# Performance work log

Measured on AMD Instinct MI355X. Metric: run time of the kernel, lower is better.

Reference implementation:

```python
import jax, jax.numpy as jnp
import numpy as np
import math

B, S, HID = 2, 2048, 2048
H, HK, D = 16, 4, 128          # query heads, kv heads, head_dim
R = 64                         # rope_dim = head_dim * partial_rotary_factor
EPS = 1e-6
THETA = 10000.0


def _rope_tables():
    inv_freq = 1.0 / (THETA ** (np.arange(0, R, 2, dtype=np.float32) / R))
    t = np.arange(S, dtype=np.float32)
    freqs = np.outer(t, inv_freq)                      # [S, R/2]
    emb = np.concatenate([freqs, freqs], axis=-1)      # [S, R]
    cos = np.broadcast_to(np.cos(emb)[None], (B, S, R)).copy()
    sin = np.broadcast_to(np.sin(emb)[None], (B, S, R)).copy()
    return jnp.asarray(cos), jnp.asarray(sin)


def setup_inputs() -> dict:
    key = jax.random.key(0)
    ks = jax.random.split(key, 3)
    cos, sin = _rope_tables()
    return {
        "hidden_states": jax.random.normal(ks[0], (B, S, HID), dtype=jnp.float32),
        "cos": cos,
        "sin": sin,
        "w_qkv": jax.random.normal(ks[1], ((H + 2 * HK) * D, HID), dtype=jnp.float32) * (HID ** -0.5),
        "q_ln_w": jnp.ones((D,), dtype=jnp.float32),
        "k_ln_w": jnp.ones((D,), dtype=jnp.float32),
        "w_dense": jax.random.normal(ks[2], (HID, H * D), dtype=jnp.float32) * ((H * D) ** -0.5),
    }


def _rms_norm(x, w):
    xf = x.astype(jnp.float32)
    var = jnp.mean(xf * xf, axis=-1, keepdims=True)
    return w * (xf * jax.lax.rsqrt(var + EPS)).astype(x.dtype)


def _rotate_half(x):
    x1, x2 = x[..., : x.shape[-1] // 2], x[..., x.shape[-1] // 2 :]
    return jnp.concatenate([-x2, x1], axis=-1)


def _apply_rope(q, k, cos, sin):
    # cos/sin: [B, S, R] -> [B, 1, S, R]; partial rotary on first R dims
    cos = cos[:, None, :, :]
    sin = sin[:, None, :, :]
    q_rot, q_pass = q[..., :R], q[..., R:]
    k_rot, k_pass = k[..., :R], k[..., R:]
    q_emb = q_rot * cos + _rotate_half(q_rot) * sin
    k_emb = k_rot * cos + _rotate_half(k_rot) * sin
    return (jnp.concatenate([q_emb, q_pass], axis=-1),
            jnp.concatenate([k_emb, k_pass], axis=-1))


def reference(hidden_states, cos, sin, w_qkv, q_ln_w, k_ln_w, w_dense):
    bsz, q_len, _ = hidden_states.shape
    qkv = jnp.einsum('bsh,oh->bso', hidden_states, w_qkv)            # [B,S,(H+2HK)*D]
    qkv = qkv.reshape(bsz, q_len, H + 2 * HK, D)
    q, k, v = jnp.split(qkv, [H, H + HK], axis=2)
    q = jnp.transpose(q, (0, 2, 1, 3))                               # [B,H,S,D]
    k = jnp.transpose(k, (0, 2, 1, 3))                               # [B,HK,S,D]
    v = jnp.transpose(v, (0, 2, 1, 3))

    q = _rms_norm(q, q_ln_w)
    k = _rms_norm(k, k_ln_w)
    q, k = _apply_rope(q, k, cos, sin)

    n_rep = H // HK
    k = jnp.repeat(k, n_rep, axis=1)                                 # [B,H,S,D]
    v = jnp.repeat(v, n_rep, axis=1)

    scores = jnp.einsum('bhqd,bhkd->bhqk', q, k) / math.sqrt(D)
    probs = jax.nn.softmax(scores.astype(jnp.float32), axis=-1).astype(q.dtype)
    attn = jnp.einsum('bhqk,bhkd->bhqd', probs, v)                   # [B,H,S,D]
    attn = jnp.transpose(attn, (0, 2, 1, 3)).reshape(bsz, q_len, H * D)
    return jnp.einsum('bsd,od->bso', attn, w_dense)                  # [B,S,HID]
```

## Files before the change

kernel.cpp:

```cpp
#include <hip/hip_runtime.h>
#include <hip/hip_bf16.h>
#include <math.h>

#define B_   2
#define S_   2048
#define HID_ 2048
#define H_   16
#define HK_  4
#define D_   128
#define NH_  24
#define QKVN 3072
#define R_   64

typedef __attribute__((ext_vector_type(8))) _Float16 h8;
typedef __attribute__((ext_vector_type(4))) _Float16 h4;
typedef __attribute__((ext_vector_type(2))) _Float16 h2;
typedef __attribute__((ext_vector_type(4))) float f4;

#define GLOAD16(gp, lp) __builtin_amdgcn_global_load_lds(                      \
    (const __attribute__((address_space(1))) void*)(gp),                       \
    (__attribute__((address_space(3))) void*)(lp), 16, 0, 0)

__global__ __launch_bounds__(256) void cvt3(
    const float* __restrict__ s0, _Float16* __restrict__ d0, int n0,
    const float* __restrict__ s1, _Float16* __restrict__ d1, int n1,
    const float* __restrict__ s2, _Float16* __restrict__ d2, int n2)
{
    int j = blockIdx.x * 256 + threadIdx.x;
    const float* s; _Float16* d;
    if (j < n0) { s = s0; d = d0; }
    else {
        j -= n0;
        if (j < n1) { s = s1; d = d1; }
        else { j -= n1; if (j >= n2) return; s = s2; d = d2; }
    }
    float4 a = ((const float4*)s)[j * 2];
    float4 b = ((const float4*)s)[j * 2 + 1];
    h8 h;
    h[0] = (_Float16)a.x; h[1] = (_Float16)a.y;
    h[2] = (_Float16)a.z; h[3] = (_Float16)a.w;
    h[4] = (_Float16)b.x; h[5] = (_Float16)b.y;
    h[6] = (_Float16)b.z; h[7] = (_Float16)b.w;
    ((h8*)d)[j] = h;
}

__global__ __launch_bounds__(256) void gemm_qkv(
    const _Float16* __restrict__ A, const _Float16* __restrict__ Bm,
    const float* __restrict__ cosT, const float* __restrict__ sinT,
    const float* __restrict__ qw, const float* __restrict__ kw,
    _Float16* __restrict__ Qh_g, _Float16* __restrict__ Kh_g,
    _Float16* __restrict__ Vt_g)
{
    __shared__ _Float16 smem[2][128][64];
    __shared__ float exch[2][128];
    auto Ast = smem[0];
    auto Bst = smem[1];

    const int tid = threadIdx.x;
    const int wave = tid >> 6, lane = tid & 63;
    const int l15 = lane & 15, l4 = lane >> 4;
    const int h  = blockIdx.x;
    const int m0 = blockIdx.y * 128;
    const int n0 = h * 128;
    const int wm = (wave >> 1) * 64, wn = (wave & 1) * 64;
    const int K = HID_;

    f4 acc[16];
#pragma unroll
    for (int t = 0; t < 16; ++t) acc[t] = (f4){0.f, 0.f, 0.f, 0.f};

    const int srow = lane >> 3;
    const int scol = ((lane & 7) ^ srow) * 8;
    const int sw   = l15 & 7;

    for (int k0 = 0; k0 < K; k0 += 64) {
        __syncthreads();
#pragma unroll
        for (int t = 0; t < 4; ++t) {
            const int chunk = wave * 4 + t;
            const int grow  = chunk * 8 + srow;
            GLOAD16(A  + (size_t)(m0 + grow) * K + k0 + scol, &Ast[chunk * 8][0]);
            GLOAD16(Bm + (size_t)(n0 + grow) * K + k0 + scol, &Bst[chunk * 8][0]);
        }
        __syncthreads();

#pragma unroll
        for (int j = 0; j < 2; ++j) {
            h8 ahf[4], bhf[4];
#pragma unroll
            for (int i = 0; i < 4; ++i) {
                ahf[i] = *(const h8*)&Ast[wm + i * 16 + l15][((j * 4 + l4) ^ sw) * 8];
                bhf[i] = *(const h8*)&Bst[wn + i * 16 + l15][((j * 4 + l4) ^ sw) * 8];
            }
            __builtin_amdgcn_s_setprio(1);
#pragma unroll
            for (int i = 0; i < 4; ++i)
#pragma unroll
                for (int jj = 0; jj < 4; ++jj)
                    acc[i * 4 + jj] = __builtin_amdgcn_mfma_f32_16x16x32_f16(
                        ahf[i], bhf[jj], acc[i * 4 + jj], 0, 0, 0);
            __builtin_amdgcn_s_setprio(0);
        }
    }

    const int bb = m0 >> 11;
    const int s0 = m0 & 2047;

    if (h < 20) {
        float sq[4][4];
#pragma unroll
        for (int i = 0; i < 4; ++i)
#pragma unroll
            for (int r = 0; r < 4; ++r) {
                float s = 0.f;
#pragma unroll
                for (int jj = 0; jj < 4; ++jj) {
                    float v = acc[i * 4 + jj][r];
                    s += v * v;
                }
                s += __shfl_xor(s, 1);
                s += __shfl_xor(s, 2);
                s += __shfl_xor(s, 4);
                s += __shfl_xor(s, 8);
                sq[i][r] = s;
            }
        const int half = wn >> 6;
        if (l15 == 0) {
#pragma unroll
            for (int i = 0; i < 4; ++i)
#pragma unroll
                for (int r = 0; r < 4; ++r)
                    exch[half][wm + i * 16 + l4 * 4 + r] = sq[i][r];
        }
        __syncthreads();

        const float* wln = (h < 16) ? qw : kw;
        float wv[4];
#pragma unroll
        for (int jj = 0; jj < 4; ++jj) wv[jj] = wln[wn + jj * 16 + l15];

        const float QS = 0.08838834764831845f * 1.4426950408889634f;
        _Float16 (*Ld)[128] = (_Float16 (*)[128])smem;

#pragma unroll
        for (int i = 0; i < 4; ++i) {
#pragma unroll
            for (int r = 0; r < 4; ++r) {
                const int row = wm + i * 16 + l4 * 4 + r;
                const int s  = s0 + row;
                float tot = sq[i][r] + exch[half ^ 1][row];
                float scale = rsqrtf(tot * (1.f / 128.f) + 1e-6f);
                float y[4];
#pragma unroll
                for (int jj = 0; jj < 4; ++jj)
                    y[jj] = acc[i * 4 + jj][r] * scale * wv[jj];

                float yr[4];
                if (wn == 0) {
                    const float* cp = cosT + ((size_t)bb * S_ + s) * R_;
                    const float* sp = sinT + ((size_t)bb * S_ + s) * R_;
                    float cs[4], sn[4];
#pragma unroll
                    for (int jj = 0; jj < 4; ++jj) {
                        cs[jj] = cp[jj * 16 + l15];
                        sn[jj] = sp[jj * 16 + l15];
                    }
                    yr[0] = y[0] * cs[0] - y[2] * sn[0];
                    yr[1] = y[1] * cs[1] - y[3] * sn[1];
                    yr[2] = y[2] * cs[2] + y[0] * sn[2];
                    yr[3] = y[3] * cs[3] + y[1] * sn[3];
                } else {
#pragma unroll
                    for (int jj = 0; jj < 4; ++jj) yr[jj] = y[jj];
                }

                const float os = (h < 16) ? QS : 1.f;
#pragma unroll
                for (int jj = 0; jj < 4; ++jj)
                    Ld[row][wn + jj * 16 + l15] = (_Float16)(yr[jj] * os);
            }
        }
        __syncthreads();

        _Float16* outb = (h < 16)
            ? Qh_g + (((size_t)bb * H_ + h) * S_ + s0) * D_
            : Kh_g + (((size_t)bb * HK_ + (h - 16)) * S_ + s0) * D_;
        const int rr = tid >> 4;
        const int d0 = (tid & 15) * 8;
#pragma unroll
        for (int it = 0; it < 8; ++it) {
            const int row = it * 16 + rr;
            *(h8*)(outb + (size_t)row * D_ + d0) = *(const h8*)&Ld[row][d0];
        }
    } else {
        const size_t vbase = ((size_t)bb * HK_ + (h - 20)) * D_ * S_;
#pragma unroll
        for (int i = 0; i < 4; ++i)
#pragma unroll
            for (int jj = 0; jj < 4; ++jj) {
                h4 pk;
#pragma unroll
                for (int r = 0; r < 4; ++r) pk[r] = (_Float16)acc[i * 4 + jj][r];
                const int d = wn + jj * 16 + l15;
                const int s = s0 + wm + i * 16 + l4 * 4;
                *(h4*)(Vt_g + vbase + (size_t)d * S_ + s) = pk;
            }
    }
}

__global__ __launch_bounds__(256) void gemm_dense(
    const _Float16* __restrict__ A, const _Float16* __restrict__ Bm,
    float* __restrict__ Cv, int M, int N, int K)
{
    __shared__ _Float16 Ast[128][64];
    __shared__ _Float16 Bst[128][64];

    const int tid = threadIdx.x;
    const int wave = tid >> 6, lane = tid & 63;
    const int l15 = lane & 15, l4 = lane >> 4;
    const int m0 = blockIdx.y * 128, n0 = blockIdx.x * 128;
    const int wm = (wave >> 1) * 64, wn = (wave & 1) * 64;

    f4 acc[16];
#pragma unroll
    for (int t = 0; t < 16; ++t) acc[t] = (f4){0.f, 0.f, 0.f, 0.f};

    const int srow = lane >> 3;
    const int scol = ((lane & 7) ^ srow) * 8;
    const int sw   = l15 & 7;

    for (int k0 = 0; k0 < K; k0 += 64) {
        __syncthreads();
#pragma unroll
        for (int t = 0; t < 4; ++t) {
            const int chunk = wave * 4 + t;
            const int grow  = chunk * 8 + srow;
            GLOAD16(A  + (size_t)(m0 + grow) * K + k0 + scol, &Ast[chunk * 8][0]);
            GLOAD16(Bm + (size_t)(n0 + grow) * K + k0 + scol, &Bst[chunk * 8][0]);
        }
        __syncthreads();

#pragma unroll
        for (int j = 0; j < 2; ++j) {
            h8 ahf[4], bhf[4];
#pragma unroll
            for (int i = 0; i < 4; ++i) {
                ahf[i] = *(const h8*)&Ast[wm + i * 16 + l15][((j * 4 + l4) ^ sw) * 8];
                bhf[i] = *(const h8*)&Bst[wn + i * 16 + l15][((j * 4 + l4) ^ sw) * 8];
            }
            __builtin_amdgcn_s_setprio(1);
#pragma unroll
            for (int i = 0; i < 4; ++i)
#pragma unroll
                for (int jj = 0; jj < 4; ++jj)
                    acc[i * 4 + jj] = __builtin_amdgcn_mfma_f32_16x16x32_f16(
                        ahf[i], bhf[jj], acc[i * 4 + jj], 0, 0, 0);
            __builtin_amdgcn_s_setprio(0);
        }
    }

#pragma unroll
    for (int i = 0; i < 4; ++i)
#pragma unroll
        for (int jj = 0; jj < 4; ++jj)
#pragma unroll
            for (int r = 0; r < 4; ++r) {
                int row = m0 + wm + i * 16 + l4 * 4 + r;
                int col = n0 + wn + jj * 16 + l15;
                Cv[(size_t)row * N + col] = acc[i * 4 + jj][r];
            }
}

__global__ __launch_bounds__(256, 2) void flash_mfma(
    const _Float16* __restrict__ Qh_g, const _Float16* __restrict__ Kh_g,
    const _Float16* __restrict__ Vt_g, _Float16* __restrict__ Ao, int bbase)
{
    __shared__ _Float16 Ksh[2][64][128];
    __shared__ _Float16 Vsh[2][128][64];
    __shared__ _Float16 Ps [128][64];

    const int tid = threadIdx.x;
    const int wave = tid >> 6, lane = tid & 63;
    const int l15 = lane & 15, l4 = lane >> 4;
    const int qb = blockIdx.x, h = blockIdx.y, b = bbase;
    const int kh = h >> 2;
    const int key = l15 & 7;

    h8 qf[2][4];
#pragma unroll
    for (int i = 0; i < 2; ++i) {
        const _Float16* qrow = Qh_g +
            (((size_t)b * H_ + h) * S_ + qb * 128 + wave * 32 + i * 16 + l15) * D_;
#pragma unroll
        for (int j = 0; j < 4; ++j)
            qf[i][j] = *(const h8*)(qrow + j * 32 + l4 * 8);
    }

    f4 o[2][8];
#pragma unroll
    for (int i = 0; i < 2; ++i)
#pragma unroll
        for (int t = 0; t < 8; ++t) o[i][t] = (f4){0.f, 0.f, 0.f, 0.f};
    float l_part[2] = {0.f, 0.f};

    const size_t kvoff = ((size_t)b * HK_ + kh) * S_ * D_;
    const _Float16* kg = Kh_g + kvoff;
    const _Float16* vg = Vt_g + kvoff;

    int krow[4], ksrc[4], vrow[4], vsrc[4];
#pragma unroll
    for (int t = 0; t < 4; ++t) {
        krow[t] = wave * 16 + t * 4 + (lane >> 4);
        ksrc[t] = ((lane & 15) ^ (krow[t] & 7)) * 8;
        vrow[t] = wave * 32 + t * 8 + (lane >> 3);
        vsrc[t] = ((lane & 7) ^ (vrow[t] & 7)) * 8;
    }

    auto STAGE = [&](int bf, int kb) {
#pragma unroll
        for (int t = 0; t < 4; ++t)
            GLOAD16(kg + (size_t)(kb * 64 + krow[t]) * D_ + ksrc[t],
                    &Ksh[bf][wave * 16 + t * 4][0]);
#pragma unroll
        for (int t = 0; t < 4; ++t)
            GLOAD16(vg + (size_t)vrow[t] * S_ + kb * 64 + vsrc[t],
                    &Vsh[bf][wave * 32 + t * 8][0]);
    };

    STAGE(0, 0);
    int cur = 0;

    for (int kb = 0; kb < S_ / 64; ++kb) {
        __syncthreads();
        if (kb + 1 < S_ / 64) STAGE(cur ^ 1, kb + 1);

        f4 acc[4][2];
#pragma unroll
        for (int c = 0; c < 4; ++c)
#pragma unroll
            for (int i = 0; i < 2; ++i)
                acc[c][i] = (f4){-8.f, -8.f, -8.f, -8.f};
#pragma unroll
        for (int j = 0; j < 4; ++j) {
#pragma unroll
            for (int c = 0; c < 4; ++c) {
                h8 kf = *(const h8*)&Ksh[cur][c * 16 + l15][((j * 4 + l4) ^ key) * 8];
#pragma unroll
                for (int i = 0; i < 2; ++i)
                    acc[c][i] = __builtin_amdgcn_mfma_f32_16x16x32_f16(
                        kf, qf[i][j], acc[c][i], 0, 0, 0);
            }
        }

#pragma unroll
        for (int c = 0; c < 4; ++c) {
#pragma unroll
            for (int i = 0; i < 2; ++i) {
                h4 pk;
#pragma unroll
                for (int r = 0; r < 4; ++r) {
                    float e_ = exp2f(acc[c][i][r]);
                    l_part[i] += e_;
                    pk[r] = (_Float16)e_;
                }
                int g = 2 * c + (l4 >> 1);
                *(h4*)&Ps[wave * 32 + i * 16 + l15][(g ^ key) * 8 + (l4 & 1) * 4] = pk;
            }
        }

#pragma unroll
        for (int s2 = 0; s2 < 2; ++s2) {
            int gc = ((s2 * 4 + l4) ^ key) * 8;
            h8 pf0 = *(const h8*)&Ps[wave * 32 + l15][gc];
            h8 pf1 = *(const h8*)&Ps[wave * 32 + 16 + l15][gc];
#pragma unroll
            for (int t = 0; t < 8; ++t) {
                h8 vf = *(const h8*)&Vsh[cur][t * 16 + l15][gc];
                o[0][t] = __builtin_amdgcn_mfma_f32_16x16x32_f16(pf0, vf, o[0][t], 0, 0, 0);
                o[1][t] = __builtin_amdgcn_mfma_f32_16x16x32_f16(pf1, vf, o[1][t], 0, 0, 0);
            }
        }
        cur ^= 1;
    }

    float Linv[2];
#pragma unroll
    for (int i = 0; i < 2; ++i) {
        float l = l_part[i];
        l += __shfl_xor(l, 16);
        l += __shfl_xor(l, 32);
        Linv[i] = 1.f / l;
    }
#pragma unroll
    for (int i = 0; i < 2; ++i) {
        float inv[4];
#pragma unroll
        for (int r = 0; r < 4; ++r) inv[r] = __shfl(Linv[i], l4 * 4 + r);
#pragma unroll
        for (int t = 0; t < 8; ++t) {
#pragma unroll
            for (int r = 0; r < 4; ++r) {
                int row = qb * 128 + wave * 32 + i * 16 + l4 * 4 + r;
                Ao[((size_t)b * S_ + row) * (H_ * D_) + h * D_ + t * 16 + l15] =
                    (_Float16)(o[i][t][r] * inv[r]);
            }
        }
    }
}

extern "C" void kernel_launch(void* const* d_in, const int* in_sizes, int n_in,
                              void* d_out, int out_size, void* d_ws, size_t ws_size,
                              hipStream_t stream)
{
    const float* hidden  = (const float*)d_in[0];
    const float* cosT    = (const float*)d_in[1];
    const float* sinT    = (const float*)d_in[2];
    const float* w_qkv   = (const float*)d_in[3];
    const float* q_ln    = (const float*)d_in[4];
    const float* k_ln    = (const float*)d_in[5];
    const float* w_dense = (const float*)d_in[6];
    float* out = (float*)d_out;

    char* w = (char*)d_ws;
    _Float16* attn16   = (_Float16*)w;
    _Float16* hidden16 = (_Float16*)(w + 16777216);
    _Float16* wqkv16   = (_Float16*)(w + 33554432);
    _Float16* Qh       = (_Float16*)(w + 46137344);
    _Float16* Kh       = (_Float16*)(w + 62914560);
    _Float16* Vt       = (_Float16*)(w + 67108864);
    _Float16* wdense16 = (_Float16*)(w + 71303168);

    cvt3<<<9216, 256, 0, stream>>>(hidden,  hidden16, 1048576,
                                   w_qkv,   wqkv16,   786432,
                                   w_dense, wdense16, 524288);

    gemm_qkv<<<dim3(NH_, (B_ * S_) / 128), 256, 0, stream>>>(
        hidden16, wqkv16, cosT, sinT, q_ln, k_ln, Qh, Kh, Vt);

    flash_mfma<<<dim3(S_ / 128, H_), 256, 0, stream>>>(Qh, Kh, Vt, attn16, 0);
    flash_mfma<<<dim3(S_ / 128, H_), 256, 0, stream>>>(Qh, Kh, Vt, attn16, 1);

    gemm_dense<<<dim3(HID_ / 128, (B_ * S_) / 128), 256, 0, stream>>>(
        attn16, wdense16, out, B_ * S_, HID_, H_ * D_);
}
```

Before: 375.3 us.

## Double-buffer LDS tiles in both GEMMs and merge flash launches over batch

Both GEMM kernels now keep two LDS buffers and issue the global-to-LDS loads for the next K tile before computing on the current one, so load latency can overlap with the MFMA work and one barrier per iteration is dropped. The two per-batch flash attention launches are merged into a single launch with batch as grid z, which doubles the blocks available to fill the GPU and removes one launch. The cost is twice the LDS per GEMM block (64KB), which may reduce occupancy.

```diff
diff --git a/kernel.cpp b/kernel.cpp
--- a/kernel.cpp
+++ b/kernel.cpp
@@ -51,10 +51,9 @@
     _Float16* __restrict__ Qh_g, _Float16* __restrict__ Kh_g,
     _Float16* __restrict__ Vt_g)
 {
-    __shared__ _Float16 smem[2][128][64];
+    __shared__ _Float16 Ast[2][128][64];
+    __shared__ _Float16 Bst[2][128][64];
     __shared__ float exch[2][128];
-    auto Ast = smem[0];
-    auto Bst = smem[1];
 
     const int tid = threadIdx.x;
     const int wave = tid >> 6, lane = tid & 63;
@@ -73,24 +72,30 @@
     const int scol = ((lane & 7) ^ srow) * 8;
     const int sw   = l15 & 7;
 
-    for (int k0 = 0; k0 < K; k0 += 64) {
-        __syncthreads();
+    auto STAGE = [&](int bf, int k0) {
 #pragma unroll
         for (int t = 0; t < 4; ++t) {
             const int chunk = wave * 4 + t;
             const int grow  = chunk * 8 + srow;
-            GLOAD16(A  + (size_t)(m0 + grow) * K + k0 + scol, &Ast[chunk * 8][0]);
-            GLOAD16(Bm + (size_t)(n0 + grow) * K + k0 + scol, &Bst[chunk * 8][0]);
-        }
+            GLOAD16(A  + (size_t)(m0 + grow) * K + k0 + scol, &Ast[bf][chunk * 8][0]);
+            GLOAD16(Bm + (size_t)(n0 + grow) * K + k0 + scol, &Bst[bf][chunk * 8][0]);
+        }
+    };
+
+    STAGE(0, 0);
+    int cur = 0;
+
+    for (int k0 = 0; k0 < K; k0 += 64) {
         __syncthreads();
+        if (k0 + 64 < K) STAGE(cur ^ 1, k0 + 64);
 
 #pragma unroll
         for (int j = 0; j < 2; ++j) {
             h8 ahf[4], bhf[4];
 #pragma unroll
             for (int i = 0; i < 4; ++i) {
-                ahf[i] = *(const h8*)&Ast[wm + i * 16 + l15][((j * 4 + l4) ^ sw) * 8];
-                bhf[i] = *(const h8*)&Bst[wn + i * 16 + l15][((j * 4 + l4) ^ sw) * 8];
+                ahf[i] = *(const h8*)&Ast[cur][wm + i * 16 + l15][((j * 4 + l4) ^ sw) * 8];
+                bhf[i] = *(const h8*)&Bst[cur][wn + i * 16 + l15][((j * 4 + l4) ^ sw) * 8];
             }
             __builtin_amdgcn_s_setprio(1);
 #pragma unroll
@@ -101,6 +106,7 @@
                         ahf[i], bhf[jj], acc[i * 4 + jj], 0, 0, 0);
             __builtin_amdgcn_s_setprio(0);
         }
+        cur ^= 1;
     }
 
     const int bb = m0 >> 11;
@@ -140,7 +146,7 @@
         for (int jj = 0; jj < 4; ++jj) wv[jj] = wln[wn + jj * 16 + l15];
 
         const float QS = 0.08838834764831845f * 1.4426950408889634f;
-        _Float16 (*Ld)[128] = (_Float16 (*)[128])smem;
+        _Float16 (*Ld)[128] = (_Float16 (*)[128])&Ast[0][0][0];
 
 #pragma unroll
         for (int i = 0; i < 4; ++i) {
@@ -212,8 +218,8 @@
     const _Float16* __restrict__ A, const _Float16* __restrict__ Bm,
     float* __restrict__ Cv, int M, int N, int K)
 {
-    __shared__ _Float16 Ast[128][64];
-    __shared__ _Float16 Bst[128][64];
+    __shared__ _Float16 Ast[2][128][64];
+    __shared__ _Float16 Bst[2][128][64];
 
     const int tid = threadIdx.x;
     const int wave = tid >> 6, lane = tid & 63;
@@ -229,24 +235,30 @@
     const int scol = ((lane & 7) ^ srow) * 8;
     const int sw   = l15 & 7;
 
-    for (int k0 = 0; k0 < K; k0 += 64) {
-        __syncthreads();
+    auto STAGE = [&](int bf, int k0) {
 #pragma unroll
         for (int t = 0; t < 4; ++t) {
             const int chunk = wave * 4 + t;
             const int grow  = chunk * 8 + srow;
-            GLOAD16(A  + (size_t)(m0 + grow) * K + k0 + scol, &Ast[chunk * 8][0]);
-            GLOAD16(Bm + (size_t)(n0 + grow) * K + k0 + scol, &Bst[chunk * 8][0]);
-        }
+            GLOAD16(A  + (size_t)(m0 + grow) * K + k0 + scol, &Ast[bf][chunk * 8][0]);
+            GLOAD16(Bm + (size_t)(n0 + grow) * K + k0 + scol, &Bst[bf][chunk * 8][0]);
+        }
+    };
+
+    STAGE(0, 0);
+    int cur = 0;
+
+    for (int k0 = 0; k0 < K; k0 += 64) {
         __syncthreads();
+        if (k0 + 64 < K) STAGE(cur ^ 1, k0 + 64);
 
 #pragma unroll
         for (int j = 0; j < 2; ++j) {
             h8 ahf[4], bhf[4];
 #pragma unroll
             for (int i = 0; i < 4; ++i) {
-                ahf[i] = *(const h8*)&Ast[wm + i * 16 + l15][((j * 4 + l4) ^ sw) * 8];
-                bhf[i] = *(const h8*)&Bst[wn + i * 16 + l15][((j * 4 + l4) ^ sw) * 8];
+                ahf[i] = *(const h8*)&Ast[cur][wm + i * 16 + l15][((j * 4 + l4) ^ sw) * 8];
+                bhf[i] = *(const h8*)&Bst[cur][wn + i * 16 + l15][((j * 4 + l4) ^ sw) * 8];
             }
             __builtin_amdgcn_s_setprio(1);
 #pragma unroll
@@ -257,6 +269,7 @@
                         ahf[i], bhf[jj], acc[i * 4 + jj], 0, 0, 0);
             __builtin_amdgcn_s_setprio(0);
         }
+        cur ^= 1;
     }
 
 #pragma unroll
@@ -273,7 +286,7 @@
 
 __global__ __launch_bounds__(256, 2) void flash_mfma(
     const _Float16* __restrict__ Qh_g, const _Float16* __restrict__ Kh_g,
-    const _Float16* __restrict__ Vt_g, _Float16* __restrict__ Ao, int bbase)
+    const _Float16* __restrict__ Vt_g, _Float16* __restrict__ Ao)
 {
     __shared__ _Float16 Ksh[2][64][128];
     __shared__ _Float16 Vsh[2][128][64];
@@ -282,7 +295,7 @@
     const int tid = threadIdx.x;
     const int wave = tid >> 6, lane = tid & 63;
     const int l15 = lane & 15, l4 = lane >> 4;
-    const int qb = blockIdx.x, h = blockIdx.y, b = bbase;
+    const int qb = blockIdx.x, h = blockIdx.y, b = blockIdx.z;
     const int kh = h >> 2;
     const int key = l15 & 7;
 
@@ -437,8 +450,7 @@
     gemm_qkv<<<dim3(NH_, (B_ * S_) / 128), 256, 0, stream>>>(
         hidden16, wqkv16, cosT, sinT, q_ln, k_ln, Qh, Kh, Vt);
 
-    flash_mfma<<<dim3(S_ / 128, H_), 256, 0, stream>>>(Qh, Kh, Vt, attn16, 0);
-    flash_mfma<<<dim3(S_ / 128, H_), 256, 0, stream>>>(Qh, Kh, Vt, attn16, 1);
+    flash_mfma<<<dim3(S_ / 128, H_, B_), 256, 0, stream>>>(Qh, Kh, Vt, attn16);
 
     gemm_dense<<<dim3(HID_ / 128, (B_ * S_) / 128), 256, 0, stream>>>(
         attn16, wdense16, out, B_ * S_, HID_, H_ * D_);
```

Measured after the change: 323.1 us. -13.9%, faster.
